# Performance work log

Hardware: AMD Instinct MI355X
Metric: run time of the kernel (lower is better)

Reference implementation:

```python
import jax, jax.numpy as jnp
import numpy as np

NUM_SEGMENTS = 100000


def setup_inputs() -> dict:
    key = jax.random.key(0)
    k1, k2 = jax.random.split(key)
    x = jax.random.normal(k1, (4000000, 32), dtype=jnp.float32)
    index = jax.random.randint(k2, (4000000,), 0, NUM_SEGMENTS, dtype=jnp.int64)
    return {"x": x, "index": index}


def reference(x, index):
    # scatter_mean(x, index, dim=0): sum rows per segment, divide by count (clamped to 1)
    sums = jax.ops.segment_sum(x, index, num_segments=NUM_SEGMENTS)  # [S, D]
    counts = jax.ops.segment_sum(jnp.ones((x.shape[0],), dtype=x.dtype), index,
                                 num_segments=NUM_SEGMENTS)  # [S]
    return sums / jnp.maximum(counts, 1.0)[:, None]
```

## Files before the change

### kernel.cpp

```cpp
#include <hip/hip_runtime.h>

#define NSEG 100000
#define DIM 32
#define NBUCKET 500
#define SEG_PER_BKT 200
#define RPB 8192
#define PTHREADS 256
#define RTHREADS 1024
#define CHUNK 2048
#define SUMSTRIDE 33

__global__ void p1_block_hist(const int* __restrict__ idx,
                              int* __restrict__ blockhist,
                              int n_rows, int nblk) {
    __shared__ int hist[NBUCKET];
    int t = threadIdx.x, blk = blockIdx.x;
    for (int i = t; i < NBUCKET; i += PTHREADS) hist[i] = 0;
    __syncthreads();
    int base = blk * RPB;
#pragma unroll
    for (int it = 0; it < RPB / PTHREADS; ++it) {
        int row = base + it * PTHREADS + t;
        if (row < n_rows) atomicAdd(&hist[idx[row] / SEG_PER_BKT], 1);
    }
    __syncthreads();
    for (int i = t; i < NBUCKET; i += PTHREADS)
        blockhist[(size_t)i * nblk + blk] = hist[i];
}

__global__ void p2_scan_blocks(int* __restrict__ blockhist,
                               int* __restrict__ totals, int nblk) {
    int bkt = blockIdx.x;
    int lane = threadIdx.x;
    int* rowp = blockhist + (size_t)bkt * nblk;
    int cpl = (nblk + 63) / 64;
    int s0 = lane * cpl;
    int s1 = min(nblk, s0 + cpl);
    int csum = 0;
    for (int i = s0; i < s1; ++i) csum += rowp[i];
    int v = csum;
    for (int d = 1; d < 64; d <<= 1) {
        int u = __shfl_up(v, d, 64);
        if (lane >= d) v += u;
    }
    int run = v - csum;
    for (int i = s0; i < s1; ++i) {
        int h = rowp[i];
        rowp[i] = run;
        run += h;
    }
    int tot = __shfl(v, 63, 64);
    if (lane == 0) totals[bkt] = tot;
}

__global__ void p3_scan_buckets(const int* __restrict__ totals,
                                int* __restrict__ bucket_base) {
    int lane = threadIdx.x;
    const int cpl = (NBUCKET + 63) / 64;
    int s0 = lane * cpl;
    int s1 = min(NBUCKET, s0 + cpl);
    int csum = 0;
    for (int i = s0; i < s1; ++i) csum += totals[i];
    int v = csum;
    for (int d = 1; d < 64; d <<= 1) {
        int u = __shfl_up(v, d, 64);
        if (lane >= d) v += u;
    }
    int run = v - csum;
    for (int i = s0; i < s1; ++i) {
        bucket_base[i] = run;
        run += totals[i];
    }
    if (lane == 63) bucket_base[NBUCKET] = v;
}

__global__ void __launch_bounds__(PTHREADS)
p4_partition(const int* __restrict__ idx,
             const int* __restrict__ blockhist,
             const int* __restrict__ bucket_base,
             unsigned int* __restrict__ perm,
             int n_rows, int nblk) {
    __shared__ int scanb[NBUCKET + 1];
    __shared__ int cnt[NBUCKET];
    __shared__ unsigned int buf[RPB];
    int t = threadIdx.x, blk = blockIdx.x;
    int base = blk * RPB;
    int rows_blk = min(RPB, n_rows - base);

    for (int i = t; i < NBUCKET; i += PTHREADS) cnt[i] = 0;
    __syncthreads();

    int segs[RPB / PTHREADS];
#pragma unroll
    for (int it = 0; it < RPB / PTHREADS; ++it) {
        int lr = it * PTHREADS + t;
        int seg = -1;
        if (lr < rows_blk) {
            seg = idx[base + lr];
            atomicAdd(&cnt[seg / SEG_PER_BKT], 1);
        }
        segs[it] = seg;
    }
    __syncthreads();

    if (t < 64) {
        const int cpl = (NBUCKET + 63) / 64;
        int s0 = t * cpl, s1 = min(NBUCKET, s0 + cpl);
        int csum = 0;
        for (int i = s0; i < s1; ++i) csum += cnt[i];
        int v = csum;
        for (int d = 1; d < 64; d <<= 1) {
            int u = __shfl_up(v, d, 64);
            if (t >= d) v += u;
        }
        int run = v - csum;
        for (int i = s0; i < s1; ++i) {
            scanb[i] = run;
            run += cnt[i];
        }
        if (t == 63) scanb[NBUCKET] = v;
    }
    __syncthreads();
    for (int i = t; i < NBUCKET; i += PTHREADS) cnt[i] = 0;
    __syncthreads();

#pragma unroll
    for (int it = 0; it < RPB / PTHREADS; ++it) {
        int seg = segs[it];
        if (seg >= 0) {
            int b = seg / SEG_PER_BKT;
            int slot = scanb[b] + atomicAdd(&cnt[b], 1);
            buf[slot] = ((unsigned int)seg << 13) |
                        (unsigned int)(it * PTHREADS + t);
        }
    }
    __syncthreads();

    for (int s = t; s < rows_blk; s += PTHREADS) {
        unsigned int e = buf[s];
        int seg = (int)(e >> 13);
        int lr  = (int)(e & 8191u);
        int b   = seg / SEG_PER_BKT;
        int ls  = seg - b * SEG_PER_BKT;
        int gpos = bucket_base[b] + blockhist[(size_t)b * nblk + blk]
                 + (s - scanb[b]);
        perm[gpos] = ((unsigned int)ls << 24) | (unsigned int)(base + lr);
    }
}

__global__ void __launch_bounds__(RTHREADS)
p5_bucket_reduce(const float* __restrict__ x,
                 const unsigned int* __restrict__ perm,
                 const int* __restrict__ bucket_base,
                 float* __restrict__ out) {
    __shared__ float sums[SEG_PER_BKT * SUMSTRIDE];
    __shared__ int cnts[SEG_PER_BKT];
    __shared__ unsigned int pbuf[2][CHUNK];
    int t = threadIdx.x;
    int b = blockIdx.x;
    for (int i = t; i < SEG_PER_BKT * SUMSTRIDE; i += RTHREADS) sums[i] = 0.0f;
    for (int i = t; i < SEG_PER_BKT; i += RTHREADS) cnts[i] = 0;

    int start = bucket_base[b];
    int end   = bucket_base[b + 1];
    int total = end - start;

    const float4* x4 = (const float4*)x;
    int g   = t >> 3;
    int sub = t & 7;

    int m0 = min(CHUNK, total);
    for (int i = t; i < m0; i += RTHREADS) pbuf[0][i] = perm[start + i];
    __syncthreads();

    int nchunks = (total + CHUNK - 1) / CHUNK;
    for (int c = 0; c < nchunks; ++c) {
        int cb  = start + c * CHUNK;
        int m   = min(CHUNK, end - cb);
        int cur = c & 1, nxt = cur ^ 1;

        unsigned int r0 = 0, r1 = 0;
        int nm = 0;
        if (c + 1 < nchunks) {
            int nb = cb + CHUNK;
            nm = min(CHUNK, end - nb);
            if (t < nm)          r0 = perm[nb + t];
            if (t + 1024 < nm)   r1 = perm[nb + t + 1024];
        }

        int i = g;
        for (; i + 384 < m; i += 512) {
            unsigned int e0 = pbuf[cur][i];
            unsigned int e1 = pbuf[cur][i + 128];
            unsigned int e2 = pbuf[cur][i + 256];
            unsigned int e3 = pbuf[cur][i + 384];
            float4 v0 = x4[(size_t)(e0 & 0xFFFFFFu) * 8 + sub];
            float4 v1 = x4[(size_t)(e1 & 0xFFFFFFu) * 8 + sub];
            float4 v2 = x4[(size_t)(e2 & 0xFFFFFFu) * 8 + sub];
            float4 v3 = x4[(size_t)(e3 & 0xFFFFFFu) * 8 + sub];
            int s0 = (int)(e0 >> 24) * SUMSTRIDE + sub * 4;
            int s1 = (int)(e1 >> 24) * SUMSTRIDE + sub * 4;
            int s2 = (int)(e2 >> 24) * SUMSTRIDE + sub * 4;
            int s3 = (int)(e3 >> 24) * SUMSTRIDE + sub * 4;
            atomicAdd(&sums[s0 + 0], v0.x); atomicAdd(&sums[s0 + 1], v0.y);
            atomicAdd(&sums[s0 + 2], v0.z); atomicAdd(&sums[s0 + 3], v0.w);
            atomicAdd(&sums[s1 + 0], v1.x); atomicAdd(&sums[s1 + 1], v1.y);
            atomicAdd(&sums[s1 + 2], v1.z); atomicAdd(&sums[s1 + 3], v1.w);
            atomicAdd(&sums[s2 + 0], v2.x); atomicAdd(&sums[s2 + 1], v2.y);
            atomicAdd(&sums[s2 + 2], v2.z); atomicAdd(&sums[s2 + 3], v2.w);
            atomicAdd(&sums[s3 + 0], v3.x); atomicAdd(&sums[s3 + 1], v3.y);
            atomicAdd(&sums[s3 + 2], v3.z); atomicAdd(&sums[s3 + 3], v3.w);
            if (sub == 0) {
                atomicAdd(&cnts[e0 >> 24], 1);
                atomicAdd(&cnts[e1 >> 24], 1);
                atomicAdd(&cnts[e2 >> 24], 1);
                atomicAdd(&cnts[e3 >> 24], 1);
            }
        }
        for (; i < m; i += 128) {
            unsigned int e = pbuf[cur][i];
            float4 v = x4[(size_t)(e & 0xFFFFFFu) * 8 + sub];
            int s0 = (int)(e >> 24) * SUMSTRIDE + sub * 4;
            atomicAdd(&sums[s0 + 0], v.x); atomicAdd(&sums[s0 + 1], v.y);
            atomicAdd(&sums[s0 + 2], v.z); atomicAdd(&sums[s0 + 3], v.w);
            if (sub == 0) atomicAdd(&cnts[e >> 24], 1);
        }

        if (c + 1 < nchunks) {
            if (t < nm)        pbuf[nxt][t] = r0;
            if (t + 1024 < nm) pbuf[nxt][t + 1024] = r1;
        }
        __syncthreads();
    }

    for (int e = t; e < SEG_PER_BKT * DIM; e += RTHREADS) {
        int ls  = e >> 5;
        int col = e & 31;
        float cf = (float)cnts[ls];
        out[(size_t)b * SEG_PER_BKT * DIM + e] =
            sums[ls * SUMSTRIDE + col] / fmaxf(cf, 1.0f);
    }
}

__global__ void scatter_sum_kernel(const float* __restrict__ x,
                                   const int* __restrict__ idx,
                                   float* __restrict__ sums,
                                   float* __restrict__ cnts,
                                   int n_elems) {
    int i = blockIdx.x * blockDim.x + threadIdx.x;
    if (i >= n_elems) return;
    int row = i >> 5;
    int col = i & 31;
    int seg = idx[row];
    atomicAdd(&sums[seg * DIM + col], x[i]);
    if (col == 0) atomicAdd(&cnts[seg], 1.0f);
}

__global__ void divide_kernel(float* __restrict__ out,
                              const float* __restrict__ cnts, int n) {
    int i = blockIdx.x * blockDim.x + threadIdx.x;
    if (i >= n) return;
    float c = cnts[i >> 5];
    out[i] = out[i] / fmaxf(c, 1.0f);
}


extern "C" void kernel_launch(void* const* d_in, const int* in_sizes, int n_in,
                              void* d_out, int out_size, void* d_ws, size_t ws_size,
                              hipStream_t stream) {
    const float* x   = (const float*)d_in[0];
    const int*   idx = (const int*)d_in[1];
    float* out = (float*)d_out;

    int n_elems = in_sizes[0];
    int n_rows  = n_elems / DIM;
    int nblk    = (n_rows + RPB - 1) / RPB;

    size_t need = ((size_t)n_rows + (size_t)NBUCKET * nblk + NBUCKET + NBUCKET + 1)
                  * sizeof(int);

    if (ws_size >= need && n_rows <= (1 << 24)) {
        unsigned int* perm = (unsigned int*)d_ws;
        int* blockhist   = (int*)(perm + n_rows);
        int* totals      = blockhist + (size_t)NBUCKET * nblk;
        int* bucket_base = totals + NBUCKET;

        p1_block_hist<<<nblk, PTHREADS, 0, stream>>>(idx, blockhist, n_rows, nblk);
        p2_scan_blocks<<<NBUCKET, 64, 0, stream>>>(blockhist, totals, nblk);
        p3_scan_buckets<<<1, 64, 0, stream>>>(totals, bucket_base);
        p4_partition<<<nblk, PTHREADS, 0, stream>>>(idx, blockhist, bucket_base,
                                                    perm, n_rows, nblk);
        p5_bucket_reduce<<<NBUCKET, RTHREADS, 0, stream>>>(x, perm, bucket_base, out);
    } else {
        float* cnts = (float*)d_ws;
        hipMemsetAsync(d_out, 0, (size_t)out_size * sizeof(float), stream);
        hipMemsetAsync(d_ws, 0, (size_t)NSEG * sizeof(float), stream);

        const int threads = 256;
        int blocks = (n_elems + threads - 1) / threads;
        scatter_sum_kernel<<<blocks, threads, 0, stream>>>(x, idx, out, cnts, n_elems);
        int blocks2 = (out_size + threads - 1) / threads;
        divide_kernel<<<blocks2, threads, 0, stream>>>(out, cnts, out_size);
    }
}
```

Before: 1.229 ms.

## Split gather into row windows with cache-prefetch pass per window

Partitions rows into buckets crossed with four row windows, so each gather pass only reads rows from one quarter of x. Before each pass a streaming kernel reads that window sequentially, aiming to warm the large last-level cache so the random gathers that follow hit in cache. The histogram and scan stages are also simplified: a global atomic histogram and a single scan replace the per-block histogram and two scans, and partition offsets are claimed with global atomic cursors. In exchange the whole of x is read twice, partial sums are round-tripped through out and a count buffer between passes, the extra launches add overhead, and the order of rows within a partition is no longer deterministic.

```diff
diff --git a/kernel.cpp b/kernel.cpp
--- a/kernel.cpp
+++ b/kernel.cpp
@@ -4,40 +4,42 @@
 #define DIM 32
 #define NBUCKET 500
 #define SEG_PER_BKT 200
+#define NWIN 4
+#define NPART (NBUCKET * NWIN)
 #define RPB 8192
 #define PTHREADS 256
 #define RTHREADS 1024
 #define CHUNK 2048
 #define SUMSTRIDE 33
 
-__global__ void p1_block_hist(const int* __restrict__ idx,
-                              int* __restrict__ blockhist,
-                              int n_rows, int nblk) {
-    __shared__ int hist[NBUCKET];
+__global__ void q1_hist(const int* __restrict__ idx, int* __restrict__ gtot,
+                        int n_rows, int wrows) {
+    __shared__ int hist[NPART];
     int t = threadIdx.x, blk = blockIdx.x;
-    for (int i = t; i < NBUCKET; i += PTHREADS) hist[i] = 0;
+    for (int i = t; i < NPART; i += PTHREADS) hist[i] = 0;
     __syncthreads();
     int base = blk * RPB;
-#pragma unroll
     for (int it = 0; it < RPB / PTHREADS; ++it) {
         int row = base + it * PTHREADS + t;
-        if (row < n_rows) atomicAdd(&hist[idx[row] / SEG_PER_BKT], 1);
-    }
-    __syncthreads();
-    for (int i = t; i < NBUCKET; i += PTHREADS)
-        blockhist[(size_t)i * nblk + blk] = hist[i];
-}
-
-__global__ void p2_scan_blocks(int* __restrict__ blockhist,
-                               int* __restrict__ totals, int nblk) {
-    int bkt = blockIdx.x;
+        if (row < n_rows) {
+            int seg = idx[row];
+            int p = (seg / SEG_PER_BKT) * NWIN + row / wrows;
+            atomicAdd(&hist[p], 1);
+        }
+    }
+    __syncthreads();
+    for (int i = t; i < NPART; i += PTHREADS)
+        if (hist[i]) atomicAdd(&gtot[i], hist[i]);
+}
+
+__global__ void q2_scan(const int* __restrict__ gtot,
+                        int* __restrict__ part_base,
+                        int* __restrict__ gcursor) {
     int lane = threadIdx.x;
-    int* rowp = blockhist + (size_t)bkt * nblk;
-    int cpl = (nblk + 63) / 64;
-    int s0 = lane * cpl;
-    int s1 = min(nblk, s0 + cpl);
+    const int cpl = (NPART + 63) / 64;
+    int s0 = lane * cpl, s1 = min(NPART, s0 + cpl);
     int csum = 0;
-    for (int i = s0; i < s1; ++i) csum += rowp[i];
+    for (int i = s0; i < s1; ++i) csum += gtot[i];
     int v = csum;
     for (int d = 1; d < 64; d <<= 1) {
         int u = __shfl_up(v, d, 64);
@@ -45,69 +47,40 @@
     }
     int run = v - csum;
     for (int i = s0; i < s1; ++i) {
-        int h = rowp[i];
-        rowp[i] = run;
-        run += h;
-    }
-    int tot = __shfl(v, 63, 64);
-    if (lane == 0) totals[bkt] = tot;
-}
-
-__global__ void p3_scan_buckets(const int* __restrict__ totals,
-                                int* __restrict__ bucket_base) {
-    int lane = threadIdx.x;
-    const int cpl = (NBUCKET + 63) / 64;
-    int s0 = lane * cpl;
-    int s1 = min(NBUCKET, s0 + cpl);
-    int csum = 0;
-    for (int i = s0; i < s1; ++i) csum += totals[i];
-    int v = csum;
-    for (int d = 1; d < 64; d <<= 1) {
-        int u = __shfl_up(v, d, 64);
-        if (lane >= d) v += u;
-    }
-    int run = v - csum;
-    for (int i = s0; i < s1; ++i) {
-        bucket_base[i] = run;
-        run += totals[i];
-    }
-    if (lane == 63) bucket_base[NBUCKET] = v;
+        part_base[i] = run;
+        gcursor[i] = run;
+        run += gtot[i];
+    }
+    if (lane == 63) part_base[NPART] = v;
 }
 
 __global__ void __launch_bounds__(PTHREADS)
-p4_partition(const int* __restrict__ idx,
-             const int* __restrict__ blockhist,
-             const int* __restrict__ bucket_base,
-             unsigned int* __restrict__ perm,
-             int n_rows, int nblk) {
-    __shared__ int scanb[NBUCKET + 1];
-    __shared__ int cnt[NBUCKET];
+q3_partition(const int* __restrict__ idx, int* __restrict__ gcursor,
+             unsigned int* __restrict__ perm, int n_rows, int wrows) {
+    __shared__ int idxb[RPB];
     __shared__ unsigned int buf[RPB];
+    __shared__ int hist[NPART];
+    __shared__ int scanb[NPART];
+    __shared__ int runb[NPART];
     int t = threadIdx.x, blk = blockIdx.x;
     int base = blk * RPB;
     int rows_blk = min(RPB, n_rows - base);
 
-    for (int i = t; i < NBUCKET; i += PTHREADS) cnt[i] = 0;
-    __syncthreads();
-
-    int segs[RPB / PTHREADS];
-#pragma unroll
-    for (int it = 0; it < RPB / PTHREADS; ++it) {
-        int lr = it * PTHREADS + t;
-        int seg = -1;
-        if (lr < rows_blk) {
-            seg = idx[base + lr];
-            atomicAdd(&cnt[seg / SEG_PER_BKT], 1);
-        }
-        segs[it] = seg;
+    for (int i = t; i < NPART; i += PTHREADS) hist[i] = 0;
+    for (int i = t; i < rows_blk; i += PTHREADS) idxb[i] = idx[base + i];
+    __syncthreads();
+
+    for (int i = t; i < rows_blk; i += PTHREADS) {
+        int p = (idxb[i] / SEG_PER_BKT) * NWIN + (base + i) / wrows;
+        atomicAdd(&hist[p], 1);
     }
     __syncthreads();
 
     if (t < 64) {
-        const int cpl = (NBUCKET + 63) / 64;
-        int s0 = t * cpl, s1 = min(NBUCKET, s0 + cpl);
+        const int cpl = (NPART + 63) / 64;
+        int s0 = t * cpl, s1 = min(NPART, s0 + cpl);
         int csum = 0;
-        for (int i = s0; i < s1; ++i) csum += cnt[i];
+        for (int i = s0; i < s1; ++i) csum += hist[i];
         int v = csum;
         for (int d = 1; d < 64; d <<= 1) {
             int u = __shfl_up(v, d, 64);
@@ -116,23 +89,22 @@
         int run = v - csum;
         for (int i = s0; i < s1; ++i) {
             scanb[i] = run;
-            run += cnt[i];
-        }
-        if (t == 63) scanb[NBUCKET] = v;
-    }
-    __syncthreads();
-    for (int i = t; i < NBUCKET; i += PTHREADS) cnt[i] = 0;
-    __syncthreads();
-
-#pragma unroll
-    for (int it = 0; it < RPB / PTHREADS; ++it) {
-        int seg = segs[it];
-        if (seg >= 0) {
-            int b = seg / SEG_PER_BKT;
-            int slot = scanb[b] + atomicAdd(&cnt[b], 1);
-            buf[slot] = ((unsigned int)seg << 13) |
-                        (unsigned int)(it * PTHREADS + t);
-        }
+            run += hist[i];
+        }
+    }
+    __syncthreads();
+
+    for (int i = t; i < NPART; i += PTHREADS) {
+        int c = hist[i];
+        if (c > 0) runb[i] = atomicAdd(&gcursor[i], c);
+    }
+    __syncthreads();
+
+    for (int i = t; i < rows_blk; i += PTHREADS) {
+        int seg = idxb[i];
+        int p = (seg / SEG_PER_BKT) * NWIN + (base + i) / wrows;
+        int r = atomicSub(&hist[p], 1) - 1;
+        buf[scanb[p] + r] = ((unsigned int)seg << 13) | (unsigned int)i;
     }
     __syncthreads();
 
@@ -140,60 +112,63 @@
         unsigned int e = buf[s];
         int seg = (int)(e >> 13);
         int lr  = (int)(e & 8191u);
+        int row = base + lr;
         int b   = seg / SEG_PER_BKT;
-        int ls  = seg - b * SEG_PER_BKT;
-        int gpos = bucket_base[b] + blockhist[(size_t)b * nblk + blk]
-                 + (s - scanb[b]);
-        perm[gpos] = ((unsigned int)ls << 24) | (unsigned int)(base + lr);
-    }
+        int p   = b * NWIN + row / wrows;
+        int gpos = runb[p] + (s - scanb[p]);
+        perm[gpos] = ((unsigned int)(seg - b * SEG_PER_BKT) << 24) |
+                     (unsigned int)row;
+    }
+}
+
+__global__ void touch_window(const float4* __restrict__ x4,
+                             long long f4_begin, long long f4_end) {
+    long long stride = (long long)gridDim.x * blockDim.x;
+    long long i = (long long)blockIdx.x * blockDim.x + threadIdx.x + f4_begin;
+    float acc = 0.0f;
+    for (; i < f4_end; i += stride) {
+        float4 v = x4[i];
+        acc += v.x + v.y + v.z + v.w;
+    }
+    asm volatile("" :: "v"(acc));
 }
 
 __global__ void __launch_bounds__(RTHREADS)
-p5_bucket_reduce(const float* __restrict__ x,
-                 const unsigned int* __restrict__ perm,
-                 const int* __restrict__ bucket_base,
-                 float* __restrict__ out) {
+g5_gather(const float* __restrict__ x, const unsigned int* __restrict__ perm,
+          const int* __restrict__ part_base, float* __restrict__ out,
+          int* __restrict__ gcnt, int w) {
     __shared__ float sums[SEG_PER_BKT * SUMSTRIDE];
-    __shared__ int cnts[SEG_PER_BKT];
-    __shared__ unsigned int pbuf[2][CHUNK];
-    int t = threadIdx.x;
-    int b = blockIdx.x;
-    for (int i = t; i < SEG_PER_BKT * SUMSTRIDE; i += RTHREADS) sums[i] = 0.0f;
-    for (int i = t; i < SEG_PER_BKT; i += RTHREADS) cnts[i] = 0;
-
-    int start = bucket_base[b];
-    int end   = bucket_base[b + 1];
-    int total = end - start;
+    __shared__ int cntl[SEG_PER_BKT];
+    __shared__ unsigned int pbuf[CHUNK];
+    int t = threadIdx.x, b = blockIdx.x;
+
+    if (w == 0) {
+        for (int i = t; i < SEG_PER_BKT * SUMSTRIDE; i += RTHREADS) sums[i] = 0.0f;
+        for (int i = t; i < SEG_PER_BKT; i += RTHREADS) cntl[i] = 0;
+    } else {
+        for (int e = t; e < SEG_PER_BKT * DIM; e += RTHREADS)
+            sums[(e >> 5) * SUMSTRIDE + (e & 31)] =
+                out[(size_t)b * SEG_PER_BKT * DIM + e];
+        for (int i = t; i < SEG_PER_BKT; i += RTHREADS)
+            cntl[i] = gcnt[b * SEG_PER_BKT + i];
+    }
+    int start = part_base[b * NWIN + w];
+    int end   = part_base[b * NWIN + w + 1];
+    __syncthreads();
 
     const float4* x4 = (const float4*)x;
-    int g   = t >> 3;
-    int sub = t & 7;
-
-    int m0 = min(CHUNK, total);
-    for (int i = t; i < m0; i += RTHREADS) pbuf[0][i] = perm[start + i];
-    __syncthreads();
-
-    int nchunks = (total + CHUNK - 1) / CHUNK;
-    for (int c = 0; c < nchunks; ++c) {
-        int cb  = start + c * CHUNK;
-        int m   = min(CHUNK, end - cb);
-        int cur = c & 1, nxt = cur ^ 1;
-
-        unsigned int r0 = 0, r1 = 0;
-        int nm = 0;
-        if (c + 1 < nchunks) {
-            int nb = cb + CHUNK;
-            nm = min(CHUNK, end - nb);
-            if (t < nm)          r0 = perm[nb + t];
-            if (t + 1024 < nm)   r1 = perm[nb + t + 1024];
-        }
-
+    int g = t >> 3, sub = t & 7;
+
+    for (int cb = start; cb < end; cb += CHUNK) {
+        int m = min(CHUNK, end - cb);
+        for (int i = t; i < m; i += RTHREADS) pbuf[i] = perm[cb + i];
+        __syncthreads();
         int i = g;
         for (; i + 384 < m; i += 512) {
-            unsigned int e0 = pbuf[cur][i];
-            unsigned int e1 = pbuf[cur][i + 128];
-            unsigned int e2 = pbuf[cur][i + 256];
-            unsigned int e3 = pbuf[cur][i + 384];
+            unsigned int e0 = pbuf[i];
+            unsigned int e1 = pbuf[i + 128];
+            unsigned int e2 = pbuf[i + 256];
+            unsigned int e3 = pbuf[i + 384];
             float4 v0 = x4[(size_t)(e0 & 0xFFFFFFu) * 8 + sub];
             float4 v1 = x4[(size_t)(e1 & 0xFFFFFFu) * 8 + sub];
             float4 v2 = x4[(size_t)(e2 & 0xFFFFFFu) * 8 + sub];
@@ -211,34 +186,36 @@
             atomicAdd(&sums[s3 + 0], v3.x); atomicAdd(&sums[s3 + 1], v3.y);
             atomicAdd(&sums[s3 + 2], v3.z); atomicAdd(&sums[s3 + 3], v3.w);
             if (sub == 0) {
-                atomicAdd(&cnts[e0 >> 24], 1);
-                atomicAdd(&cnts[e1 >> 24], 1);
-                atomicAdd(&cnts[e2 >> 24], 1);
-                atomicAdd(&cnts[e3 >> 24], 1);
+                atomicAdd(&cntl[e0 >> 24], 1);
+                atomicAdd(&cntl[e1 >> 24], 1);
+                atomicAdd(&cntl[e2 >> 24], 1);
+                atomicAdd(&cntl[e3 >> 24], 1);
             }
         }
         for (; i < m; i += 128) {
-            unsigned int e = pbuf[cur][i];
+            unsigned int e = pbuf[i];
             float4 v = x4[(size_t)(e & 0xFFFFFFu) * 8 + sub];
             int s0 = (int)(e >> 24) * SUMSTRIDE + sub * 4;
             atomicAdd(&sums[s0 + 0], v.x); atomicAdd(&sums[s0 + 1], v.y);
             atomicAdd(&sums[s0 + 2], v.z); atomicAdd(&sums[s0 + 3], v.w);
-            if (sub == 0) atomicAdd(&cnts[e >> 24], 1);
-        }
-
-        if (c + 1 < nchunks) {
-            if (t < nm)        pbuf[nxt][t] = r0;
-            if (t + 1024 < nm) pbuf[nxt][t + 1024] = r1;
+            if (sub == 0) atomicAdd(&cntl[e >> 24], 1);
         }
         __syncthreads();
     }
 
-    for (int e = t; e < SEG_PER_BKT * DIM; e += RTHREADS) {
-        int ls  = e >> 5;
-        int col = e & 31;
-        float cf = (float)cnts[ls];
-        out[(size_t)b * SEG_PER_BKT * DIM + e] =
-            sums[ls * SUMSTRIDE + col] / fmaxf(cf, 1.0f);
+    if (w == NWIN - 1) {
+        for (int e = t; e < SEG_PER_BKT * DIM; e += RTHREADS) {
+            int ls = e >> 5, col = e & 31;
+            float cf = (float)cntl[ls];
+            out[(size_t)b * SEG_PER_BKT * DIM + e] =
+                sums[ls * SUMSTRIDE + col] / fmaxf(cf, 1.0f);
+        }
+    } else {
+        for (int e = t; e < SEG_PER_BKT * DIM; e += RTHREADS)
+            out[(size_t)b * SEG_PER_BKT * DIM + e] =
+                sums[(e >> 5) * SUMSTRIDE + (e & 31)];
+        for (int i = t; i < SEG_PER_BKT; i += RTHREADS)
+            gcnt[b * SEG_PER_BKT + i] = cntl[i];
     }
 }
 
@@ -275,22 +252,33 @@
     int n_elems = in_sizes[0];
     int n_rows  = n_elems / DIM;
     int nblk    = (n_rows + RPB - 1) / RPB;
-
-    size_t need = ((size_t)n_rows + (size_t)NBUCKET * nblk + NBUCKET + NBUCKET + 1)
+    int wrows   = (n_rows + NWIN - 1) / NWIN;
+
+    size_t need = ((size_t)n_rows + NPART + (NPART + 1) + NPART + NSEG)
                   * sizeof(int);
 
     if (ws_size >= need && n_rows <= (1 << 24)) {
         unsigned int* perm = (unsigned int*)d_ws;
-        int* blockhist   = (int*)(perm + n_rows);
-        int* totals      = blockhist + (size_t)NBUCKET * nblk;
-        int* bucket_base = totals + NBUCKET;
-
-        p1_block_hist<<<nblk, PTHREADS, 0, stream>>>(idx, blockhist, n_rows, nblk);
-        p2_scan_blocks<<<NBUCKET, 64, 0, stream>>>(blockhist, totals, nblk);
-        p3_scan_buckets<<<1, 64, 0, stream>>>(totals, bucket_base);
-        p4_partition<<<nblk, PTHREADS, 0, stream>>>(idx, blockhist, bucket_base,
-                                                    perm, n_rows, nblk);
-        p5_bucket_reduce<<<NBUCKET, RTHREADS, 0, stream>>>(x, perm, bucket_base, out);
+        int* gtot      = (int*)(perm + n_rows);
+        int* part_base = gtot + NPART;
+        int* gcursor   = part_base + NPART + 1;
+        int* gcnt      = gcursor + NPART;
+
+        hipMemsetAsync(gtot, 0, NPART * sizeof(int), stream);
+        q1_hist<<<nblk, PTHREADS, 0, stream>>>(idx, gtot, n_rows, wrows);
+        q2_scan<<<1, 64, 0, stream>>>(gtot, part_base, gcursor);
+        q3_partition<<<nblk, PTHREADS, 0, stream>>>(idx, gcursor, perm,
+                                                    n_rows, wrows);
+        const float4* x4 = (const float4*)x;
+        for (int w = 0; w < NWIN; ++w) {
+            long long rb = (long long)w * wrows;
+            long long re = rb + wrows;
+            if (re > n_rows) re = n_rows;
+            if (rb < re)
+                touch_window<<<2048, 256, 0, stream>>>(x4, rb * 8, re * 8);
+            g5_gather<<<NBUCKET, RTHREADS, 0, stream>>>(x, perm, part_base,
+                                                        out, gcnt, w);
+        }
     } else {
         float* cnts = (float*)d_ws;
         hipMemsetAsync(d_out, 0, (size_t)out_size * sizeof(float), stream);
```

Result: slower. 1.418 ms (+15.4%).
